# Kernel optimization log

Hardware: AMD Instinct MI355X
Metric: run time of the kernel (lower is better)

Reference implementation:

```python
import jax, jax.numpy as jnp
import numpy as np

N_WAY = 64

def setup_inputs() -> dict:
    key = jax.random.key(0)
    k1, k2, k3, k4 = jax.random.split(key, 4)
    S, Q, F, D = 1024, 16384, 2048, 512
    xs = jax.random.normal(k1, (S, F), dtype=jnp.float32)
    ys = jax.random.randint(k2, (S,), 0, N_WAY, dtype=jnp.int64)
    xq = jax.random.normal(k3, (Q, F), dtype=jnp.float32)
    W = jax.random.normal(k4, (F, D), dtype=jnp.float32) * 0.02
    b = jnp.zeros((D,), dtype=jnp.float32)
    return {"xs": xs, "ys": ys, "xq": xq, "W": W, "b": b}

def reference(xs, ys, xq, W, b):
    # encoder: linear projection [*, F] -> [*, D]
    z_s = xs @ W + b            # [S, D]
    z_q = xq @ W + b            # [Q, D]
    # class prototypes: segment mean over support embeddings -> [N_way, D]
    counts = jax.ops.segment_sum(jnp.ones_like(ys, dtype=z_s.dtype), ys, num_segments=N_WAY)
    proto = jax.ops.segment_sum(z_s, ys, num_segments=N_WAY) / jnp.clip(counts, 1.0)[:, None]
    # pairwise squared euclidean distance (expand + pow + sum), [Q, N_way]
    diff = z_q[:, None, :] - proto[None, :, :]   # [Q, N_way, D]
    dists = jnp.sum(diff * diff, axis=-1)
    return -dists
```

## Files before the change

### kernel.cpp

```cpp
#include <hip/hip_runtime.h>


typedef __attribute__((ext_vector_type(8))) short short8;
typedef __attribute__((ext_vector_type(4))) float floatx4;

#define S_ROWS 1024
#define F_DIM  2048
#define D_DIM  512
#define NWAY   64
#define Q_ROWS 16384

static __device__ __forceinline__ unsigned short f2bf(float f) {
  unsigned int u = __float_as_uint(f);
  u += 0x7FFF + ((u >> 16) & 1);
  return (unsigned short)(u >> 16);
}
static __device__ __forceinline__ float bf2f(unsigned short s) {
  return __uint_as_float(((unsigned int)s) << 16);
}

static __device__ __forceinline__ void load_lds16(const unsigned short* g, unsigned short* l) {
  __builtin_amdgcn_global_load_lds((const __attribute__((address_space(1))) unsigned int*)g,
                                   (__attribute__((address_space(3))) unsigned int*)l,
                                   16, 0, 0);
}

__global__ __launch_bounds__(256) void k0_transpose(const float* __restrict__ W,
                                                    unsigned short* __restrict__ Wt,
                                                    float* __restrict__ qnorm,
                                                    float* __restrict__ proto_acc) {
  __shared__ unsigned short t[64][65];
  int bx = blockIdx.x;
  int f0 = (bx >> 3) << 6;
  int d0 = (bx & 7) << 6;
  for (int j = 0; j < 16; j++) {
    int lin = j * 256 + threadIdx.x;
    int fl = lin >> 6, dl = lin & 63;
    t[fl][dl] = f2bf(W[(size_t)(f0 + fl) * 512 + d0 + dl]);
  }
  __syncthreads();
  for (int j = 0; j < 16; j++) {
    int lin = j * 256 + threadIdx.x;
    int dl = lin >> 6, fl = lin & 63;
    Wt[(size_t)(d0 + dl) * 2048 + f0 + fl] = t[fl][dl];
  }
  int tid = threadIdx.x;
  if (tid < 64) qnorm[bx * 64 + tid] = 0.f;
  else if (tid < 192) proto_acc[bx * 128 + tid - 64] = 0.f;
}

__global__ __launch_bounds__(256) void k0_sort(const int* __restrict__ ys,
                                               int* __restrict__ order,
                                               int* __restrict__ starts,
                                               float* __restrict__ counts) {
  __shared__ int cnt[NWAY];
  __shared__ int st[NWAY + 1];
  __shared__ int wp[NWAY];
  int tid = threadIdx.x;
  if (tid < NWAY) cnt[tid] = 0;
  __syncthreads();
  for (int j = tid; j < S_ROWS; j += 256) atomicAdd(&cnt[ys[j]], 1);
  __syncthreads();
  if (tid == 0) {
    int a = 0;
    for (int c = 0; c < NWAY; c++) { st[c] = a; wp[c] = a; a += cnt[c]; }
    st[NWAY] = a;
  }
  __syncthreads();
  for (int j = tid; j < S_ROWS; j += 256) {
    int c = ys[j];
    int p = atomicAdd(&wp[c], 1);
    order[p] = j;
  }
  if (tid < NWAY) counts[tid] = (float)cnt[tid];
  if (tid < NWAY + 1) starts[tid] = st[tid];
}

__global__ __launch_bounds__(256) void k1_csum(const float* __restrict__ xs,
                                               const int* __restrict__ order,
                                               const int* __restrict__ starts,
                                               float* __restrict__ csum) {
  __shared__ int lord[S_ROWS];
  int c = blockIdx.x >> 1;
  int tid = threadIdx.x;
  int s = starts[c], e = starts[c + 1];
  int len = e - s;
  for (int j = tid; j < len; j += 256) lord[j] = order[s + j];
  __syncthreads();
  int f0 = (blockIdx.x & 1) * 1024 + tid * 4;
  float4 a = {0.f, 0.f, 0.f, 0.f};
  for (int i = 0; i < len; i++) {
    float4 v = *(const float4*)&xs[(size_t)lord[i] * F_DIM + f0];
    a.x += v.x; a.y += v.y; a.z += v.z; a.w += v.w;
  }
  *(float4*)&csum[(size_t)c * F_DIM + f0] = a;
}

__global__ __launch_bounds__(256) void k2_proto(const float* __restrict__ W,
                                               const float* __restrict__ csum,
                                               float* __restrict__ proto_acc) {
  __shared__ float cs[256];
  int bx = blockIdx.x;
  int c = bx >> 4;
  int dh = ((bx >> 3) & 1) * 256;
  int fc = (bx & 7) * 256;
  int tid = threadIdx.x;
  cs[tid] = csum[(size_t)c * F_DIM + fc + tid];
  __syncthreads();
  float a0 = 0.f;
#pragma unroll 8
  for (int f = 0; f < 256; f++)
    a0 += cs[f] * W[(size_t)(fc + f) * 512 + dh + tid];
  atomicAdd(&proto_acc[c * 512 + dh + tid], a0);
}

__global__ __launch_bounds__(256) void k2b_finalize(const float* __restrict__ proto_acc,
                                                    const float* __restrict__ b,
                                                    const float* __restrict__ counts,
                                                    unsigned short* __restrict__ proto_bf,
                                                    float* __restrict__ pnorm) {
  __shared__ float red[256];
  int n = blockIdx.x, tid = threadIdx.x;
  float cntv = counts[n];
  float inv = 1.f / fmaxf(cntv, 1.f);
  float acc = 0.f;
#pragma unroll
  for (int h = 0; h < 2; h++) {
    int d = h * 256 + tid;
    float p = (proto_acc[n * 512 + d] + cntv * b[d]) * inv;
    unsigned short hh = f2bf(p);
    proto_bf[(size_t)n * 512 + d] = hh;
    float q = bf2f(hh);
    acc += q * q;
  }
  red[tid] = acc;
  __syncthreads();
  for (int s = 128; s > 0; s >>= 1) {
    if (tid < s) red[tid] += red[tid + s];
    __syncthreads();
  }
  if (tid == 0) pnorm[n] = red[0];
}

__global__ __launch_bounds__(256) void k_cvt(const float* __restrict__ xq,
                                             unsigned short* __restrict__ xqb) {
  size_t i = ((size_t)blockIdx.x * 256 + threadIdx.x) * 8;
  float4 v0 = *(const float4*)&xq[i];
  float4 v1 = *(const float4*)&xq[i + 4];
  ushort4 w0, w1;
  w0.x = f2bf(v0.x); w0.y = f2bf(v0.y); w0.z = f2bf(v0.z); w0.w = f2bf(v0.w);
  w1.x = f2bf(v1.x); w1.y = f2bf(v1.y); w1.z = f2bf(v1.z); w1.w = f2bf(v1.w);
  *(ushort4*)&xqb[i] = w0;
  *(ushort4*)&xqb[i + 4] = w1;
}

__global__ __launch_bounds__(256) void k3_gemm1_fast(const unsigned short* __restrict__ xqb,
                                                     const unsigned short* __restrict__ Wt,
                                                     const float* __restrict__ b,
                                                     unsigned short* __restrict__ zq,
                                                     float* __restrict__ qnorm) {
  __shared__ __align__(16) unsigned short lA[128 * 32];
  __shared__ __align__(16) unsigned short lB[128 * 32];
  int tid = threadIdx.x;
  int bx = blockIdx.x;
  int n0 = (bx & 3) * 128;
  int m0 = (bx >> 2) * 128;
  int wave = tid >> 6, lane = tid & 63;
  int wm = (wave & 1) * 64, wn = (wave >> 1) * 64;
  int lrow = lane & 15, lquad = lane >> 4;

  floatx4 acc[4][4];
#pragma unroll
  for (int i = 0; i < 4; i++)
#pragma unroll
    for (int j = 0; j < 4; j++) acc[i][j] = (floatx4){0.f, 0.f, 0.f, 0.f};

  int c0 = wave * 64 + lane;

  for (int k0 = 0; k0 < F_DIM; k0 += 32) {
#pragma unroll
    for (int i = 0; i < 2; i++) {
      int c = i * 256 + c0;
      int row = c >> 2, k8 = (c & 3) * 8;
      load_lds16(&xqb[(size_t)(m0 + row) * F_DIM + k0 + k8],
                 &lA[(size_t)(i * 256 + wave * 64) * 8]);
      load_lds16(&Wt[(size_t)(n0 + row) * F_DIM + k0 + k8],
                 &lB[(size_t)(i * 256 + wave * 64) * 8]);
    }
    __syncthreads();
    short8 af[4], bfr[4];
#pragma unroll
    for (int i = 0; i < 4; i++) af[i] = *(const short8*)&lA[(wm + i * 16 + lrow) * 32 + lquad * 8];
#pragma unroll
    for (int j = 0; j < 4; j++) bfr[j] = *(const short8*)&lB[(wn + j * 16 + lrow) * 32 + lquad * 8];
#pragma unroll
    for (int i = 0; i < 4; i++)
#pragma unroll
      for (int j = 0; j < 4; j++)
        acc[i][j] = __builtin_amdgcn_mfma_f32_16x16x32_bf16(af[i], bfr[j], acc[i][j], 0, 0, 0);
    __syncthreads();
  }

#pragma unroll
  for (int i = 0; i < 4; i++) {
    float rn[4] = {0.f, 0.f, 0.f, 0.f};
#pragma unroll
    for (int j = 0; j < 4; j++) {
      int col = n0 + wn + j * 16 + lrow;
      float bb = b[col];
#pragma unroll
      for (int r = 0; r < 4; r++) {
        int row = m0 + wm + i * 16 + lquad * 4 + r;
        float v = acc[i][j][r] + bb;
        unsigned short h = f2bf(v);
        zq[(size_t)row * 512 + col] = h;
        float vq = bf2f(h);
        rn[r] += vq * vq;
      }
    }
#pragma unroll
    for (int r = 0; r < 4; r++) {
      float s = rn[r];
      s += __shfl_xor(s, 1, 16);
      s += __shfl_xor(s, 2, 16);
      s += __shfl_xor(s, 4, 16);
      s += __shfl_xor(s, 8, 16);
      if (lrow == 0) {
        int row = m0 + wm + i * 16 + lquad * 4 + r;
        atomicAdd(&qnorm[row], s);
      }
    }
  }
}

__global__ __launch_bounds__(256) void k3_gemm1(const float* __restrict__ xq,
                                                const unsigned short* __restrict__ Wt,
                                                const float* __restrict__ b,
                                                unsigned short* __restrict__ zq,
                                                float* __restrict__ qnorm) {
  __shared__ unsigned short lA[128 * 32];
  __shared__ unsigned short lB[128 * 32];
  int tid = threadIdx.x;
  int bx = blockIdx.x;
  int n0 = (bx & 3) * 128;
  int m0 = (bx >> 2) * 128;
  int wave = tid >> 6, lane = tid & 63;
  int wm = (wave & 1) * 64, wn = (wave >> 1) * 64;
  int lrow = lane & 15, lquad = lane >> 4;

  floatx4 acc[4][4];
#pragma unroll
  for (int i = 0; i < 4; i++)
#pragma unroll
    for (int j = 0; j < 4; j++) acc[i][j] = (floatx4){0.f, 0.f, 0.f, 0.f};

  int a_row = tid >> 3, a_kq = tid & 7;
  int b_n = tid >> 2, b_k8 = (tid & 3) * 8;

  for (int k0 = 0; k0 < F_DIM; k0 += 32) {
#pragma unroll
    for (int p = 0; p < 4; p++) {
      int row = p * 32 + a_row;
      float4 v = *(const float4*)&xq[(size_t)(m0 + row) * F_DIM + k0 + a_kq * 4];
      ushort4 w;
      w.x = f2bf(v.x); w.y = f2bf(v.y); w.z = f2bf(v.z); w.w = f2bf(v.w);
      *(ushort4*)&lA[row * 32 + a_kq * 4] = w;
    }
#pragma unroll
    for (int p = 0; p < 2; p++) {
      int n = p * 64 + b_n;
      *(float4*)&lB[n * 32 + b_k8] = *(const float4*)&Wt[(size_t)(n0 + n) * 2048 + k0 + b_k8];
    }
    __syncthreads();
    short8 af[4], bfr[4];
#pragma unroll
    for (int i = 0; i < 4; i++) af[i] = *(const short8*)&lA[(wm + i * 16 + lrow) * 32 + lquad * 8];
#pragma unroll
    for (int j = 0; j < 4; j++) bfr[j] = *(const short8*)&lB[(wn + j * 16 + lrow) * 32 + lquad * 8];
#pragma unroll
    for (int i = 0; i < 4; i++)
#pragma unroll
      for (int j = 0; j < 4; j++)
        acc[i][j] = __builtin_amdgcn_mfma_f32_16x16x32_bf16(af[i], bfr[j], acc[i][j], 0, 0, 0);
    __syncthreads();
  }

#pragma unroll
  for (int i = 0; i < 4; i++) {
    float rn[4] = {0.f, 0.f, 0.f, 0.f};
#pragma unroll
    for (int j = 0; j < 4; j++) {
      int col = n0 + wn + j * 16 + lrow;
      float bb = b[col];
#pragma unroll
      for (int r = 0; r < 4; r++) {
        int row = m0 + wm + i * 16 + lquad * 4 + r;
        float v = acc[i][j][r] + bb;
        unsigned short h = f2bf(v);
        zq[(size_t)row * 512 + col] = h;
        float vq = bf2f(h);
        rn[r] += vq * vq;
      }
    }
#pragma unroll
    for (int r = 0; r < 4; r++) {
      float s = rn[r];
      s += __shfl_xor(s, 1, 16);
      s += __shfl_xor(s, 2, 16);
      s += __shfl_xor(s, 4, 16);
      s += __shfl_xor(s, 8, 16);
      if (lrow == 0) {
        int row = m0 + wm + i * 16 + lquad * 4 + r;
        atomicAdd(&qnorm[row], s);
      }
    }
  }
}

__global__ __launch_bounds__(256) void k4_gemm2(const unsigned short* __restrict__ zq,
                                                const unsigned short* __restrict__ proto_bf,
                                                const float* __restrict__ qnorm,
                                                const float* __restrict__ pnorm,
                                                float* __restrict__ out) {
  __shared__ unsigned short lA[128 * 32];
  __shared__ unsigned short lB[64 * 32];
  int tid = threadIdx.x;
  int r0 = blockIdx.x * 128;
  int wave = tid >> 6, lane = tid & 63;
  int lrow = lane & 15, lquad = lane >> 4;

  floatx4 acc[2][4];
#pragma unroll
  for (int i = 0; i < 2; i++)
#pragma unroll
    for (int j = 0; j < 4; j++) acc[i][j] = (floatx4){0.f, 0.f, 0.f, 0.f};

  int a_n = tid >> 2, a_k8 = (tid & 3) * 8;

  for (int k0 = 0; k0 < 512; k0 += 32) {
#pragma unroll
    for (int p = 0; p < 2; p++) {
      int row = p * 64 + a_n;
      *(float4*)&lA[row * 32 + a_k8] = *(const float4*)&zq[(size_t)(r0 + row) * 512 + k0 + a_k8];
    }
    *(float4*)&lB[a_n * 32 + a_k8] = *(const float4*)&proto_bf[(size_t)a_n * 512 + k0 + a_k8];
    __syncthreads();
    short8 af[2], bfr[4];
#pragma unroll
    for (int i = 0; i < 2; i++) af[i] = *(const short8*)&lA[(wave * 32 + i * 16 + lrow) * 32 + lquad * 8];
#pragma unroll
    for (int j = 0; j < 4; j++) bfr[j] = *(const short8*)&lB[(j * 16 + lrow) * 32 + lquad * 8];
#pragma unroll
    for (int i = 0; i < 2; i++)
#pragma unroll
      for (int j = 0; j < 4; j++)
        acc[i][j] = __builtin_amdgcn_mfma_f32_16x16x32_bf16(af[i], bfr[j], acc[i][j], 0, 0, 0);
    __syncthreads();
  }

#pragma unroll
  for (int i = 0; i < 2; i++) {
#pragma unroll
    for (int j = 0; j < 4; j++) {
      int col = j * 16 + lrow;
      float pn = pnorm[col];
#pragma unroll
      for (int r = 0; r < 4; r++) {
        int row = r0 + wave * 32 + i * 16 + lquad * 4 + r;
        out[(size_t)row * 64 + col] = 2.f * acc[i][j][r] - qnorm[row] - pn;
      }
    }
  }
}

extern "C" void kernel_launch(void* const* d_in, const int* in_sizes, int n_in,
                              void* d_out, int out_size, void* d_ws, size_t ws_size,
                              hipStream_t stream) {
  const float* xs = (const float*)d_in[0];
  const int* ys = (const int*)d_in[1];
  const float* xq = (const float*)d_in[2];
  const float* W = (const float*)d_in[3];
  const float* b = (const float*)d_in[4];
  float* out = (float*)d_out;
  char* ws = (char*)d_ws;

  size_t off = 0;
  auto take = [&](size_t bytes) -> char* {
    char* r = ws + off;
    off += (bytes + 255) & ~(size_t)255;
    return r;
  };
  unsigned short* Wt = (unsigned short*)take((size_t)D_DIM * F_DIM * 2);
  unsigned short* zq = (unsigned short*)take((size_t)Q_ROWS * D_DIM * 2);
  float* csum = (float*)take((size_t)NWAY * F_DIM * 4);
  float* proto_acc = (float*)take((size_t)NWAY * D_DIM * 4);
  unsigned short* proto_bf = (unsigned short*)take((size_t)NWAY * D_DIM * 2);
  float* qnorm = (float*)take((size_t)Q_ROWS * 4);
  float* counts = (float*)take(NWAY * 4);
  float* pnorm = (float*)take(NWAY * 4);
  int* order = (int*)take(S_ROWS * 4);
  int* starts = (int*)take((NWAY + 1) * 4);
  unsigned short* xqb = (unsigned short*)take((size_t)Q_ROWS * F_DIM * 2);
  bool fast = (off <= ws_size);

  k0_transpose<<<256, 256, 0, stream>>>(W, Wt, qnorm, proto_acc);
  k0_sort<<<1, 256, 0, stream>>>(ys, order, starts, counts);
  k1_csum<<<128, 256, 0, stream>>>(xs, order, starts, csum);
  k2_proto<<<1024, 256, 0, stream>>>(W, csum, proto_acc);
  k2b_finalize<<<64, 256, 0, stream>>>(proto_acc, b, counts, proto_bf, pnorm);
  if (fast) {
    k_cvt<<<(Q_ROWS * F_DIM) / (256 * 8), 256, 0, stream>>>(xq, xqb);
    k3_gemm1_fast<<<512, 256, 0, stream>>>(xqb, Wt, b, zq, qnorm);
  } else {
    k3_gemm1<<<512, 256, 0, stream>>>(xq, Wt, b, zq, qnorm);
  }
  k4_gemm2<<<128, 256, 0, stream>>>(zq, proto_bf, qnorm, pnorm, out);
}
```

Before: 297.6 us.

## Fuse encoder GEMM with distance GEMM via per-slice partial accumulation into output

Folds the query projection and the prototype-distance GEMM into one kernel. Each block keeps its 128x128 bf16 z tile in LDS, multiplies it by the matching 128-column slice of the prototypes, and atomically adds its partial distance (including the partial query and prototype norms) into the zero-initialised output. This removes the zq round trip through global memory, the global qnorm atomics and the separate gemm2 launch. Block indices are also remapped so each XCD works on a contiguous range of rows. The cost is four float atomics per output element from the different D slices, and the fallback path for small workspaces is dropped.

```diff
diff --git a/kernel.cpp b/kernel.cpp
--- a/kernel.cpp
+++ b/kernel.cpp
@@ -27,7 +27,7 @@
 
 __global__ __launch_bounds__(256) void k0_transpose(const float* __restrict__ W,
                                                     unsigned short* __restrict__ Wt,
-                                                    float* __restrict__ qnorm,
+                                                    float* __restrict__ outz,
                                                     float* __restrict__ proto_acc) {
   __shared__ unsigned short t[64][65];
   int bx = blockIdx.x;
@@ -45,8 +45,11 @@
     Wt[(size_t)(d0 + dl) * 2048 + f0 + fl] = t[fl][dl];
   }
   int tid = threadIdx.x;
-  if (tid < 64) qnorm[bx * 64 + tid] = 0.f;
-  else if (tid < 192) proto_acc[bx * 128 + tid - 64] = 0.f;
+  float4 zz = {0.f, 0.f, 0.f, 0.f};
+#pragma unroll
+  for (int p = 0; p < 4; p++)
+    *(float4*)&outz[(size_t)bx * 4096 + p * 1024 + tid * 4] = zz;
+  if (tid < 128) proto_acc[bx * 128 + tid] = 0.f;
 }
 
 __global__ __launch_bounds__(256) void k0_sort(const int* __restrict__ ys,
@@ -118,12 +121,12 @@
                                                     const float* __restrict__ b,
                                                     const float* __restrict__ counts,
                                                     unsigned short* __restrict__ proto_bf,
-                                                    float* __restrict__ pnorm) {
+                                                    float* __restrict__ pnorm_part) {
   __shared__ float red[256];
   int n = blockIdx.x, tid = threadIdx.x;
   float cntv = counts[n];
   float inv = 1.f / fmaxf(cntv, 1.f);
-  float acc = 0.f;
+  float qsq[2];
 #pragma unroll
   for (int h = 0; h < 2; h++) {
     int d = h * 256 + tid;
@@ -131,15 +134,20 @@
     unsigned short hh = f2bf(p);
     proto_bf[(size_t)n * 512 + d] = hh;
     float q = bf2f(hh);
-    acc += q * q;
-  }
-  red[tid] = acc;
-  __syncthreads();
-  for (int s = 128; s > 0; s >>= 1) {
-    if (tid < s) red[tid] += red[tid + s];
+    qsq[h] = q * q;
+  }
+#pragma unroll
+  for (int h = 0; h < 2; h++) {
     __syncthreads();
-  }
-  if (tid == 0) pnorm[n] = red[0];
+    red[tid] = qsq[h];
+    __syncthreads();
+    for (int s = 64; s > 0; s >>= 1) {
+      if ((tid & 127) < s) red[tid] += red[tid + s];
+      __syncthreads();
+    }
+    if (tid == 0) pnorm_part[(h * 2 + 0) * 64 + n] = red[0];
+    if (tid == 128) pnorm_part[(h * 2 + 1) * 64 + n] = red[128];
+  }
 }
 
 __global__ __launch_bounds__(256) void k_cvt(const float* __restrict__ xq,
@@ -154,17 +162,29 @@
   *(ushort4*)&xqb[i + 4] = w1;
 }
 
-__global__ __launch_bounds__(256) void k3_gemm1_fast(const unsigned short* __restrict__ xqb,
-                                                     const unsigned short* __restrict__ Wt,
-                                                     const float* __restrict__ b,
-                                                     unsigned short* __restrict__ zq,
-                                                     float* __restrict__ qnorm) {
-  __shared__ __align__(16) unsigned short lA[128 * 32];
-  __shared__ __align__(16) unsigned short lB[128 * 32];
+#define ZS_LD 136
+__global__ __launch_bounds__(256) void k3_fused(const unsigned short* __restrict__ xqb,
+                                                const unsigned short* __restrict__ Wt,
+                                                const float* __restrict__ b,
+                                                const unsigned short* __restrict__ proto_bf,
+                                                const float* __restrict__ pnorm_part,
+                                                float* __restrict__ out) {
+  __shared__ __align__(16) char smem[53248];
+  unsigned short* lA = (unsigned short*)smem;
+  unsigned short* lB = (unsigned short*)(smem + 8192);
+  unsigned short* zs = (unsigned short*)smem;
+  unsigned short* pb = (unsigned short*)(smem + 34816);
+  float* qnf = (float*)(smem + 52224);
+  float* pnl = (float*)(smem + 52736);
+
   int tid = threadIdx.x;
   int bx = blockIdx.x;
-  int n0 = (bx & 3) * 128;
-  int m0 = (bx >> 2) * 128;
+  int xcd = bx & 7;
+  int g = bx >> 3;
+  int m0 = (xcd * 16 + (g & 15)) * 128;
+  int n0 = (g >> 4) * 128;
+  int slice = g >> 4;
+
   int wave = tid >> 6, lane = tid & 63;
   int wm = (wave & 1) * 64, wn = (wave >> 1) * 64;
   int lrow = lane & 15, lquad = lane >> 4;
@@ -201,19 +221,23 @@
     __syncthreads();
   }
 
+  if (tid < 128) qnf[tid] = 0.f;
+  if (tid < 64) pnl[tid] = pnorm_part[slice * 64 + tid];
+  __syncthreads();
+
 #pragma unroll
   for (int i = 0; i < 4; i++) {
     float rn[4] = {0.f, 0.f, 0.f, 0.f};
 #pragma unroll
     for (int j = 0; j < 4; j++) {
-      int col = n0 + wn + j * 16 + lrow;
-      float bb = b[col];
+      int ld = wn + j * 16 + lrow;
+      float bb = b[n0 + ld];
 #pragma unroll
       for (int r = 0; r < 4; r++) {
-        int row = m0 + wm + i * 16 + lquad * 4 + r;
+        int rl = wm + i * 16 + lquad * 4 + r;
         float v = acc[i][j][r] + bb;
         unsigned short h = f2bf(v);
-        zq[(size_t)row * 512 + col] = h;
+        zs[rl * ZS_LD + ld] = h;
         float vq = bf2f(h);
         rn[r] += vq * vq;
       }
@@ -225,149 +249,52 @@
       s += __shfl_xor(s, 2, 16);
       s += __shfl_xor(s, 4, 16);
       s += __shfl_xor(s, 8, 16);
-      if (lrow == 0) {
-        int row = m0 + wm + i * 16 + lquad * 4 + r;
-        atomicAdd(&qnorm[row], s);
-      }
-    }
-  }
-}
-
-__global__ __launch_bounds__(256) void k3_gemm1(const float* __restrict__ xq,
-                                                const unsigned short* __restrict__ Wt,
-                                                const float* __restrict__ b,
-                                                unsigned short* __restrict__ zq,
-                                                float* __restrict__ qnorm) {
-  __shared__ unsigned short lA[128 * 32];
-  __shared__ unsigned short lB[128 * 32];
-  int tid = threadIdx.x;
-  int bx = blockIdx.x;
-  int n0 = (bx & 3) * 128;
-  int m0 = (bx >> 2) * 128;
-  int wave = tid >> 6, lane = tid & 63;
-  int wm = (wave & 1) * 64, wn = (wave >> 1) * 64;
-  int lrow = lane & 15, lquad = lane >> 4;
-
-  floatx4 acc[4][4];
-#pragma unroll
-  for (int i = 0; i < 4; i++)
-#pragma unroll
-    for (int j = 0; j < 4; j++) acc[i][j] = (floatx4){0.f, 0.f, 0.f, 0.f};
-
-  int a_row = tid >> 3, a_kq = tid & 7;
-  int b_n = tid >> 2, b_k8 = (tid & 3) * 8;
-
-  for (int k0 = 0; k0 < F_DIM; k0 += 32) {
-#pragma unroll
-    for (int p = 0; p < 4; p++) {
-      int row = p * 32 + a_row;
-      float4 v = *(const float4*)&xq[(size_t)(m0 + row) * F_DIM + k0 + a_kq * 4];
-      ushort4 w;
-      w.x = f2bf(v.x); w.y = f2bf(v.y); w.z = f2bf(v.z); w.w = f2bf(v.w);
-      *(ushort4*)&lA[row * 32 + a_kq * 4] = w;
-    }
-#pragma unroll
-    for (int p = 0; p < 2; p++) {
-      int n = p * 64 + b_n;
-      *(float4*)&lB[n * 32 + b_k8] = *(const float4*)&Wt[(size_t)(n0 + n) * 2048 + k0 + b_k8];
-    }
-    __syncthreads();
-    short8 af[4], bfr[4];
-#pragma unroll
-    for (int i = 0; i < 4; i++) af[i] = *(const short8*)&lA[(wm + i * 16 + lrow) * 32 + lquad * 8];
-#pragma unroll
-    for (int j = 0; j < 4; j++) bfr[j] = *(const short8*)&lB[(wn + j * 16 + lrow) * 32 + lquad * 8];
-#pragma unroll
-    for (int i = 0; i < 4; i++)
+      if (lrow == 0) atomicAdd(&qnf[wm + i * 16 + lquad * 4 + r], s);
+    }
+  }
+
+#pragma unroll
+  for (int p = 0; p < 4; p++) {
+    int ch = p * 256 + tid;
+    int row = ch >> 4, l8 = (ch & 15) * 8;
+    *(short8*)&pb[row * ZS_LD + l8] =
+        *(const short8*)&proto_bf[(size_t)row * 512 + n0 + l8];
+  }
+  __syncthreads();
+
+  floatx4 acc2[2][4];
+#pragma unroll
+  for (int i = 0; i < 2; i++)
+#pragma unroll
+    for (int j = 0; j < 4; j++) acc2[i][j] = (floatx4){0.f, 0.f, 0.f, 0.f};
+
+#pragma unroll
+  for (int ks = 0; ks < 4; ks++) {
+    short8 af2[2], bf2[4];
+#pragma unroll
+    for (int i = 0; i < 2; i++)
+      af2[i] = *(const short8*)&zs[(wave * 32 + i * 16 + lrow) * ZS_LD + ks * 32 + lquad * 8];
+#pragma unroll
+    for (int j = 0; j < 4; j++)
+      bf2[j] = *(const short8*)&pb[(j * 16 + lrow) * ZS_LD + ks * 32 + lquad * 8];
+#pragma unroll
+    for (int i = 0; i < 2; i++)
 #pragma unroll
       for (int j = 0; j < 4; j++)
-        acc[i][j] = __builtin_amdgcn_mfma_f32_16x16x32_bf16(af[i], bfr[j], acc[i][j], 0, 0, 0);
-    __syncthreads();
-  }
-
-#pragma unroll
-  for (int i = 0; i < 4; i++) {
-    float rn[4] = {0.f, 0.f, 0.f, 0.f};
+        acc2[i][j] = __builtin_amdgcn_mfma_f32_16x16x32_bf16(af2[i], bf2[j], acc2[i][j], 0, 0, 0);
+  }
+
+#pragma unroll
+  for (int i = 0; i < 2; i++) {
 #pragma unroll
     for (int j = 0; j < 4; j++) {
-      int col = n0 + wn + j * 16 + lrow;
-      float bb = b[col];
+      int c = j * 16 + lrow;
+      float pn = pnl[c];
 #pragma unroll
       for (int r = 0; r < 4; r++) {
-        int row = m0 + wm + i * 16 + lquad * 4 + r;
-        float v = acc[i][j][r] + bb;
-        unsigned short h = f2bf(v);
-        zq[(size_t)row * 512 + col] = h;
-        float vq = bf2f(h);
-        rn[r] += vq * vq;
-      }
-    }
-#pragma unroll
-    for (int r = 0; r < 4; r++) {
-      float s = rn[r];
-      s += __shfl_xor(s, 1, 16);
-      s += __shfl_xor(s, 2, 16);
-      s += __shfl_xor(s, 4, 16);
-      s += __shfl_xor(s, 8, 16);
-      if (lrow == 0) {
-        int row = m0 + wm + i * 16 + lquad * 4 + r;
-        atomicAdd(&qnorm[row], s);
-      }
-    }
-  }
-}
-
-__global__ __launch_bounds__(256) void k4_gemm2(const unsigned short* __restrict__ zq,
-                                                const unsigned short* __restrict__ proto_bf,
-                                                const float* __restrict__ qnorm,
-                                                const float* __restrict__ pnorm,
-                                                float* __restrict__ out) {
-  __shared__ unsigned short lA[128 * 32];
-  __shared__ unsigned short lB[64 * 32];
-  int tid = threadIdx.x;
-  int r0 = blockIdx.x * 128;
-  int wave = tid >> 6, lane = tid & 63;
-  int lrow = lane & 15, lquad = lane >> 4;
-
-  floatx4 acc[2][4];
-#pragma unroll
-  for (int i = 0; i < 2; i++)
-#pragma unroll
-    for (int j = 0; j < 4; j++) acc[i][j] = (floatx4){0.f, 0.f, 0.f, 0.f};
-
-  int a_n = tid >> 2, a_k8 = (tid & 3) * 8;
-
-  for (int k0 = 0; k0 < 512; k0 += 32) {
-#pragma unroll
-    for (int p = 0; p < 2; p++) {
-      int row = p * 64 + a_n;
-      *(float4*)&lA[row * 32 + a_k8] = *(const float4*)&zq[(size_t)(r0 + row) * 512 + k0 + a_k8];
-    }
-    *(float4*)&lB[a_n * 32 + a_k8] = *(const float4*)&proto_bf[(size_t)a_n * 512 + k0 + a_k8];
-    __syncthreads();
-    short8 af[2], bfr[4];
-#pragma unroll
-    for (int i = 0; i < 2; i++) af[i] = *(const short8*)&lA[(wave * 32 + i * 16 + lrow) * 32 + lquad * 8];
-#pragma unroll
-    for (int j = 0; j < 4; j++) bfr[j] = *(const short8*)&lB[(j * 16 + lrow) * 32 + lquad * 8];
-#pragma unroll
-    for (int i = 0; i < 2; i++)
-#pragma unroll
-      for (int j = 0; j < 4; j++)
-        acc[i][j] = __builtin_amdgcn_mfma_f32_16x16x32_bf16(af[i], bfr[j], acc[i][j], 0, 0, 0);
-    __syncthreads();
-  }
-
-#pragma unroll
-  for (int i = 0; i < 2; i++) {
-#pragma unroll
-    for (int j = 0; j < 4; j++) {
-      int col = j * 16 + lrow;
-      float pn = pnorm[col];
-#pragma unroll
-      for (int r = 0; r < 4; r++) {
-        int row = r0 + wave * 32 + i * 16 + lquad * 4 + r;
-        out[(size_t)row * 64 + col] = 2.f * acc[i][j][r] - qnorm[row] - pn;
+        int ql = wave * 32 + i * 16 + lquad * 4 + r;
+        float val = 2.f * acc2[i][j][r] - qnf[ql] - pn;
+        atomicAdd(&out[(size_t)(m0 + ql) * 64 + c], val);
       }
     }
   }
@@ -391,28 +318,20 @@
     return r;
   };
   unsigned short* Wt = (unsigned short*)take((size_t)D_DIM * F_DIM * 2);
-  unsigned short* zq = (unsigned short*)take((size_t)Q_ROWS * D_DIM * 2);
   float* csum = (float*)take((size_t)NWAY * F_DIM * 4);
   float* proto_acc = (float*)take((size_t)NWAY * D_DIM * 4);
   unsigned short* proto_bf = (unsigned short*)take((size_t)NWAY * D_DIM * 2);
-  float* qnorm = (float*)take((size_t)Q_ROWS * 4);
   float* counts = (float*)take(NWAY * 4);
-  float* pnorm = (float*)take(NWAY * 4);
+  float* pnorm_part = (float*)take(4 * NWAY * 4);
   int* order = (int*)take(S_ROWS * 4);
   int* starts = (int*)take((NWAY + 1) * 4);
   unsigned short* xqb = (unsigned short*)take((size_t)Q_ROWS * F_DIM * 2);
-  bool fast = (off <= ws_size);
-
-  k0_transpose<<<256, 256, 0, stream>>>(W, Wt, qnorm, proto_acc);
+
+  k0_transpose<<<256, 256, 0, stream>>>(W, Wt, out, proto_acc);
   k0_sort<<<1, 256, 0, stream>>>(ys, order, starts, counts);
   k1_csum<<<128, 256, 0, stream>>>(xs, order, starts, csum);
   k2_proto<<<1024, 256, 0, stream>>>(W, csum, proto_acc);
-  k2b_finalize<<<64, 256, 0, stream>>>(proto_acc, b, counts, proto_bf, pnorm);
-  if (fast) {
-    k_cvt<<<(Q_ROWS * F_DIM) / (256 * 8), 256, 0, stream>>>(xq, xqb);
-    k3_gemm1_fast<<<512, 256, 0, stream>>>(xqb, Wt, b, zq, qnorm);
-  } else {
-    k3_gemm1<<<512, 256, 0, stream>>>(xq, Wt, b, zq, qnorm);
-  }
-  k4_gemm2<<<128, 256, 0, stream>>>(zq, proto_bf, qnorm, pnorm, out);
-}
+  k2b_finalize<<<64, 256, 0, stream>>>(proto_acc, b, counts, proto_bf, pnorm_part);
+  k_cvt<<<(Q_ROWS * F_DIM) / (256 * 8), 256, 0, stream>>>(xq, xqb);
+  k3_fused<<<512, 256, 0, stream>>>(xqb, Wt, b, proto_bf, pnorm_part, out);
+}
```

Measured after the change: 299.8 us. About the same (+0.7%).
